# Kernel optimization log

Measured on AMD Instinct MI355X. Metric: run time of the kernel, lower is better.

Reference implementation:

```python
import jax, jax.numpy as jnp
import numpy as np

N, DIM, L = 65536, 128, 8


def setup_inputs() -> dict:
    rng = np.random.default_rng(0)
    # depth-consistent random tree: node 0 is root (depth 0); every other node
    # gets depth in [1, L-1] and a parent chosen uniformly among depth-1 nodes.
    depth = np.zeros(N, dtype=np.int64)
    depth[1:] = rng.integers(1, L, size=N - 1)
    depth = np.sort(depth)  # node 0 stays root; contiguous levels
    parent = np.full(N, N, dtype=np.int64)  # sentinel N for the root (dropped in segment_sum slice)
    for d in range(1, L):
        cur = np.nonzero(depth == d)[0]
        prev = np.nonzero(depth == d - 1)[0]
        parent[cur] = rng.choice(prev, size=cur.size)
    key = jax.random.key(0)
    k = jax.random.split(key, 5)
    s = 1.0 / np.sqrt(DIM)
    return {
        "x": jax.random.normal(k[0], (N, DIM), jnp.float32),
        "parent": jnp.asarray(parent),
        "depth": jnp.asarray(depth),
        "Wioux": jax.random.normal(k[1], (DIM, 3 * DIM), jnp.float32) * s,
        "Wiouh": jax.random.normal(k[2], (DIM, 3 * DIM), jnp.float32) * s,
        "Wfx": jax.random.normal(k[3], (DIM, DIM), jnp.float32) * s,
        "Wfh": jax.random.normal(k[4], (DIM, DIM), jnp.float32) * s,
        "n_levels": L,
    }


def reference(x, parent, depth, Wioux, Wiouh, Wfx, Wfh, n_levels):
    n, dim = x.shape
    xi = x @ Wioux          # [N, 3d]  precomputed input projections
    xf = x @ Wfx            # [N, d]
    pidx = jnp.minimum(parent, n - 1)  # safe gather index (root sentinel clipped; root is never a child)
    h = jnp.zeros_like(x)
    c = jnp.zeros_like(x)
    # process tree bottom-up, one depth level at a time (equivalent to the
    # torch depth-descending per-node loop since children are exactly one level deeper)
    for d in range(int(n_levels) - 1, -1, -1):
        child = depth == d + 1          # nodes that are children of level-d nodes
        cm = child[:, None]
        h_sum = jax.ops.segment_sum(jnp.where(cm, h, 0.0), parent, num_segments=n + 1)[:n]
        n_child = jax.ops.segment_sum(child.astype(x.dtype), parent, num_segments=n + 1)[:n]
        # per-child forget gate: sigmoid(fx(x[parent]) + fh(h_child))
        f = jax.nn.sigmoid(xf[pidx] + h @ Wfh)
        fc_sum = jax.ops.segment_sum(jnp.where(cm, f * c, 0.0), parent, num_segments=n + 1)[:n]
        i_, o_, u_ = jnp.split(xi + h_sum @ Wiouh, 3, axis=-1)
        c_int = fc_sum + jax.nn.sigmoid(i_) * jnp.tanh(u_)
        h_int = jax.nn.sigmoid(o_) * jnp.tanh(c_int)
        leaf = (n_child == 0)[:, None]  # leaves: h = x, c = tanh(x) (as in torch code)
        h_new = jnp.where(leaf, x, h_int)
        c_new = jnp.where(leaf, jnp.tanh(x), c_int)
        lvl = (depth == d)[:, None]
        h = jnp.where(lvl, h_new, h)
        c = jnp.where(lvl, c_new, c)
    return h
```

## Files before the change

kernel.cpp:

```cpp
#include <hip/hip_runtime.h>
#include <hip/hip_bf16.h>

#define DIM 128
#define LVL 8

typedef unsigned int u32;
typedef unsigned short u16;

using bf16x8 = __attribute__((ext_vector_type(8))) short;
using f32x4  = __attribute__((ext_vector_type(4))) float;

__device__ __forceinline__ float bf2f(u16 u) { union { u32 i; float f; } v; v.i = ((u32)u) << 16; return v.f; }
__device__ __forceinline__ u16 f2bf(float f) { __hip_bfloat16 b = __float2bfloat16(f); return *reinterpret_cast<u16*>(&b); }
__device__ __forceinline__ u32 pk2(float lo, float hi) { return (u32)f2bf(lo) | ((u32)f2bf(hi) << 16); }
__device__ __forceinline__ float sigf(float x) { return 1.f / (1.f + __expf(-x)); }
__device__ __forceinline__ float tanhfast(float x) { return 1.f - 2.f / (__expf(2.f * x) + 1.f); }

__global__ void k_levels(const int* __restrict__ depth, int n, int* __restrict__ ofs) {
  int d = threadIdx.x;
  if (d > LVL) return;
  int lo = 0, hi = n;
  while (lo < hi) { int mid = (lo + hi) >> 1; if (depth[mid] < d) lo = mid + 1; else hi = mid; }
  ofs[d] = lo;
}

__global__ void k_mark(const int* __restrict__ parent, int n, int* __restrict__ haschild) {
  int j = blockIdx.x * blockDim.x + threadIdx.x;
  if (j >= n) return;
  int p = parent[j];
  if (p >= 0 && p < n) haschild[p] = 1;
}

__global__ void k_prep(const float* __restrict__ Wioux, const float* __restrict__ Wiouh,
                       const float* __restrict__ Wfx, const float* __restrict__ Wfh,
                       u16* __restrict__ WcT, u16* __restrict__ WhT, u16* __restrict__ WfhT) {
  int i = blockIdx.x * 256 + threadIdx.x;
  if (i >= 1024 * 128) return;
  int c = i >> 7, k = i & 127;
  float v; u16* dst;
  if (c < 512) {
    v = (c < 384) ? Wioux[(size_t)k * 384 + c] : Wfx[(size_t)k * 128 + (c - 384)];
    dst = &WcT[(size_t)c * 128 + k];
  } else if (c < 896) {
    int cc = c - 512; v = Wiouh[(size_t)k * 384 + cc]; dst = &WhT[(size_t)cc * 128 + k];
  } else {
    int cc = c - 896; v = Wfh[(size_t)k * 128 + cc]; dst = &WfhT[(size_t)cc * 128 + k];
  }
  *dst = f2bf(v);
}

__global__ __launch_bounds__(256) void k_big(const float* __restrict__ x, const u16* __restrict__ WcT,
                                             const int* __restrict__ haschild, u16* __restrict__ xi, int n) {
  __shared__ __align__(16) char smem[16384 + 32768];
  char* xsb = smem;
  char* wtb = smem + 16384;
  u16* dbuf = (u16*)(smem + 16384);
  __shared__ int s_any;
  int tid = threadIdx.x;
  int wave = tid >> 6, lane = tid & 63, m = lane & 15, kg = lane >> 4;
  int row0 = blockIdx.x * 64;
  if (tid == 0) {
    int a = 0;
    for (int r = 0; r < 64 && row0 + r < n; ++r) a |= haschild[row0 + r];
    s_any = a;
  }
  __syncthreads();
  if (!s_any) return;
  for (int i = tid; i < 64 * 16; i += 256) {
    int r = i >> 4, c8 = (i & 15) * 8;
    int gr = row0 + r;
    uint4 o = make_uint4(0u, 0u, 0u, 0u);
    if (gr < n) {
      float4 a = *(const float4*)(x + (size_t)gr * DIM + c8);
      float4 b = *(const float4*)(x + (size_t)gr * DIM + c8 + 4);
      o = make_uint4(pk2(a.x, a.y), pk2(a.z, a.w), pk2(b.x, b.y), pk2(b.z, b.w));
    }
    *(uint4*)(xsb + r * 256 + ((c8 * 2) ^ ((r & 7) << 4))) = o;
  }
  int arow = wave * 16 + m;
  uint4 wreg[8];
  #pragma unroll
  for (int j = 0; j < 8; ++j) {
    int i = tid + j * 256;
    wreg[j] = *(const uint4*)(WcT + (size_t)(i >> 4) * 128 + (i & 15) * 8);
  }
  for (int ci = 0; ci < 4; ++ci) {
    __syncthreads();
    #pragma unroll
    for (int j = 0; j < 8; ++j) {
      int i = tid + j * 256;
      int cl = i >> 4, k8 = (i & 15) * 8;
      *(uint4*)(wtb + cl * 256 + ((k8 * 2) ^ ((cl & 7) << 4))) = wreg[j];
    }
    __syncthreads();
    if (ci < 3) {
      #pragma unroll
      for (int j = 0; j < 8; ++j) {
        int i = tid + j * 256;
        wreg[j] = *(const uint4*)(WcT + (size_t)((ci + 1) * 128 + (i >> 4)) * 128 + (i & 15) * 8);
      }
    }
    f32x4 acc[8];
    #pragma unroll
    for (int nt = 0; nt < 8; ++nt) acc[nt] = (f32x4){0.f, 0.f, 0.f, 0.f};
    #pragma unroll
    for (int kk = 0; kk < 4; ++kk) {
      int kbyte = kk * 64 + kg * 16;
      bf16x8 a = *(const bf16x8*)(xsb + arow * 256 + (kbyte ^ ((arow & 7) << 4)));
      #pragma unroll
      for (int nt = 0; nt < 8; ++nt) {
        int col = nt * 16 + m;
        bf16x8 b = *(const bf16x8*)(wtb + col * 256 + (kbyte ^ ((col & 7) << 4)));
        acc[nt] = __builtin_amdgcn_mfma_f32_16x16x32_bf16(a, b, acc[nt], 0, 0, 0);
      }
    }
    __syncthreads();
    #pragma unroll
    for (int nt = 0; nt < 8; ++nt)
      #pragma unroll
      for (int r = 0; r < 4; ++r)
        dbuf[(wave * 16 + kg * 4 + r) * 136 + nt * 16 + m] = f2bf(acc[nt][r]);
    __syncthreads();
    int r2 = tid >> 2, q = tid & 3;
    int gr = row0 + r2;
    if (gr < n && haschild[gr]) {
      const u16* src = dbuf + r2 * 136 + q * 32;
      u16* dst = xi + (size_t)gr * 512 + ci * 128 + q * 32;
      #pragma unroll
      for (int seg = 0; seg < 4; ++seg)
        *(uint4*)(dst + seg * 8) = *(const uint4*)(src + seg * 8);
    }
  }
}

__global__ __launch_bounds__(256) void k_level(const float* __restrict__ x,
    const u16* __restrict__ WhT, const u16* __restrict__ WfhT, const u16* __restrict__ xi,
    const int* __restrict__ haschild, const int* __restrict__ parent,
    const int* __restrict__ ofs, float* __restrict__ hout,
    float* hsum, float* fcsum, int d) {
  __shared__ __align__(16) char smem[16384 + 33792];
  char* hsb = smem;
  char* wtb = smem + 16384;
  float* dbuf = (float*)(smem + 16384);
  __shared__ int ps[64];
  __shared__ int flags[64];
  __shared__ int s_uni, s_anyp;
  int v0 = ofs[d], v1 = ofs[d + 1];
  int tid = threadIdx.x;
  int wave = tid >> 6, lane = tid & 63, m = lane & 15, kg = lane >> 4;
  int arow = wave * 16 + m;
  for (int row0 = v0 + (int)blockIdx.x * 64; row0 < v1; row0 += (int)gridDim.x * 64) {
    int nrows = min(64, v1 - row0);
    if (tid < 64) {
      flags[tid] = (tid < nrows) ? haschild[row0 + tid] : 0;
      ps[tid] = (tid < nrows) ? parent[row0 + tid] : -1;
    }
    __syncthreads();
    if (tid == 0) {
      int a = 0; for (int r = 0; r < 64; ++r) a |= flags[r];
      s_anyp = a;
      int u = 1, p0 = ps[0];
      for (int r = 1; r < nrows; ++r) if (ps[r] != p0) { u = 0; break; }
      s_uni = u;
    }
    __syncthreads();
    f32x4 acc[3][8];
    #pragma unroll
    for (int ci = 0; ci < 3; ++ci)
      #pragma unroll
      for (int nt = 0; nt < 8; ++nt) acc[ci][nt] = (f32x4){0.f, 0.f, 0.f, 0.f};
    if (s_anyp) {
      for (int i = tid; i < 64 * 16; i += 256) {
        int r = i >> 4, c8 = (i & 15) * 8;
        uint4 o = make_uint4(0u, 0u, 0u, 0u);
        if (r < nrows) {
          const float* hp = hsum + (size_t)(row0 + r) * DIM + c8;
          float4 a = *(const float4*)hp; float4 b = *(const float4*)(hp + 4);
          o = make_uint4(pk2(a.x, a.y), pk2(a.z, a.w), pk2(b.x, b.y), pk2(b.z, b.w));
        }
        *(uint4*)(hsb + r * 256 + ((c8 * 2) ^ ((r & 7) << 4))) = o;
      }
      #pragma unroll
      for (int ci = 0; ci < 3; ++ci) {
        for (int i = tid; i < 128 * 16; i += 256) {
          int cl = i >> 4, k8 = (i & 15) * 8;
          uint4 v = *(const uint4*)(WhT + (size_t)(ci * 128 + cl) * 128 + k8);
          *(uint4*)(wtb + cl * 256 + ((k8 * 2) ^ ((cl & 7) << 4))) = v;
        }
        __syncthreads();
        #pragma unroll
        for (int kk = 0; kk < 4; ++kk) {
          int kbyte = kk * 64 + kg * 16;
          bf16x8 a = *(const bf16x8*)(hsb + arow * 256 + (kbyte ^ ((arow & 7) << 4)));
          #pragma unroll
          for (int nt = 0; nt < 8; ++nt) {
            int col = nt * 16 + m;
            bf16x8 b = *(const bf16x8*)(wtb + col * 256 + (kbyte ^ ((col & 7) << 4)));
            acc[ci][nt] = __builtin_amdgcn_mfma_f32_16x16x32_bf16(a, b, acc[ci][nt], 0, 0, 0);
          }
        }
        __syncthreads();
      }
    }
    float cc[8][4];
    #pragma unroll
    for (int nt = 0; nt < 8; ++nt) {
      int col = nt * 16 + m;
      #pragma unroll
      for (int r = 0; r < 4; ++r) {
        int rl = wave * 16 + kg * 4 + r;
        int grow = row0 + rl;
        float hv = 0.f, cv = 0.f;
        if (rl < nrows) {
          bool leaf = (flags[rl] == 0);
          float xv = x[(size_t)grow * DIM + col];
          float iv = bf2f(xi[(size_t)grow * 512 + col])       + acc[0][nt][r];
          float ov = bf2f(xi[(size_t)grow * 512 + 128 + col]) + acc[1][nt][r];
          float uv = bf2f(xi[(size_t)grow * 512 + 256 + col]) + acc[2][nt][r];
          float fcv = fcsum[(size_t)grow * DIM + col];
          float ci_ = fcv + sigf(iv) * tanhfast(uv);
          hv = leaf ? xv : sigf(ov) * tanhfast(ci_);
          cv = leaf ? tanhfast(xv) : ci_;
          hout[(size_t)grow * DIM + col] = hv;
        }
        cc[nt][r] = cv;
        if (d > 0) *(u16*)(hsb + rl * 256 + ((2 * col) ^ ((rl & 7) << 4))) = f2bf(hv);
      }
    }
    if (d > 0) {
      for (int i = tid; i < 128 * 16; i += 256) {
        int cl = i >> 4, k8 = (i & 15) * 8;
        uint4 v = *(const uint4*)(WfhT + (size_t)cl * 128 + k8);
        *(uint4*)(wtb + cl * 256 + ((k8 * 2) ^ ((cl & 7) << 4))) = v;
      }
      __syncthreads();
      f32x4 fp[8];
      #pragma unroll
      for (int nt = 0; nt < 8; ++nt) fp[nt] = (f32x4){0.f, 0.f, 0.f, 0.f};
      #pragma unroll
      for (int kk = 0; kk < 4; ++kk) {
        int kbyte = kk * 64 + kg * 16;
        bf16x8 a = *(const bf16x8*)(hsb + arow * 256 + (kbyte ^ ((arow & 7) << 4)));
        #pragma unroll
        for (int nt = 0; nt < 8; ++nt) {
          int col = nt * 16 + m;
          bf16x8 b = *(const bf16x8*)(wtb + col * 256 + (kbyte ^ ((col & 7) << 4)));
          fp[nt] = __builtin_amdgcn_mfma_f32_16x16x32_bf16(a, b, fp[nt], 0, 0, 0);
        }
      }
      __syncthreads();
      if (s_uni) {
        int p = ps[0];
        #pragma unroll
        for (int nt = 0; nt < 8; ++nt) {
          int col = nt * 16 + m;
          float xfv = bf2f(xi[(size_t)p * 512 + 384 + col]);
          #pragma unroll
          for (int r = 0; r < 4; ++r) {
            int rl = wave * 16 + kg * 4 + r;
            float fc = (rl < nrows) ? sigf(xfv + fp[nt][r]) * cc[nt][r] : 0.f;
            dbuf[rl * 132 + col] = fc;
          }
        }
        __syncthreads();
        if (tid < 128) {
          float sh = 0.f, sf = 0.f;
          for (int r = 0; r < 64; ++r) {
            sh += bf2f(*(const u16*)(hsb + r * 256 + ((2 * tid) ^ ((r & 7) << 4))));
            sf += dbuf[r * 132 + tid];
          }
          atomicAdd(&hsum[(size_t)p * DIM + tid], sh);
          atomicAdd(&fcsum[(size_t)p * DIM + tid], sf);
        }
        __syncthreads();
      } else {
        #pragma unroll
        for (int nt = 0; nt < 8; ++nt) {
          int col = nt * 16 + m;
          #pragma unroll
          for (int r = 0; r < 4; ++r) {
            int rl = wave * 16 + kg * 4 + r;
            if (rl < nrows) {
              int p = ps[rl];
              float xfv = bf2f(xi[(size_t)p * 512 + 384 + col]);
              float fc = sigf(xfv + fp[nt][r]) * cc[nt][r];
              atomicAdd(&fcsum[(size_t)p * DIM + col], fc);
              float hvv = bf2f(*(const u16*)(hsb + rl * 256 + ((2 * col) ^ ((rl & 7) << 4))));
              atomicAdd(&hsum[(size_t)p * DIM + col], hvv);
            }
          }
        }
        __syncthreads();
      }
    } else {
      __syncthreads();
    }
  }
}

extern "C" void kernel_launch(void* const* d_in, const int* in_sizes, int n_in,
                              void* d_out, int out_size, void* d_ws, size_t ws_size,
                              hipStream_t stream) {
  const float* x    = (const float*)d_in[0];
  const int* parent = (const int*)d_in[1];
  const int* depth  = (const int*)d_in[2];
  const float* Wioux = (const float*)d_in[3];
  const float* Wiouh = (const float*)d_in[4];
  const float* Wfx   = (const float*)d_in[5];
  const float* Wfh   = (const float*)d_in[6];
  int n = in_sizes[0] / DIM;
  float* h = (float*)d_out;

  u16*   WcT  = (u16*)d_ws;
  u16*   WhT  = WcT + 512 * 128;
  u16*   WfhT = WhT + 384 * 128;
  u16*   xi   = WfhT + 128 * 128;
  float* hsum = (float*)(xi + (size_t)n * 512);
  float* fcsum = hsum + (size_t)n * DIM;
  int*   haschild = (int*)(fcsum + (size_t)n * DIM);
  int*   ofs  = haschild + n;

  hipMemsetAsync(hsum, 0, (size_t)2 * n * DIM * sizeof(float) + (size_t)n * sizeof(int), stream);
  k_prep<<<512, 256, 0, stream>>>(Wioux, Wiouh, Wfx, Wfh, WcT, WhT, WfhT);
  k_levels<<<1, 32, 0, stream>>>(depth, n, ofs);
  k_mark<<<(n + 255) / 256, 256, 0, stream>>>(parent, n, haschild);
  k_big<<<(n + 63) / 64, 256, 0, stream>>>(x, WcT, haschild, xi, n);

  for (int d = LVL - 1; d >= 0; --d)
    k_level<<<256, 256, 0, stream>>>(x, WhT, WfhT, xi, haschild, parent, ofs, h, hsum, fcsum, d);
}
```

Baseline: 389.9 us.

## Count child degrees to replace memset with selective zeroing and direct single-child writes

Replaces the haschild flags with per-node child counts. The full memset of hsum/fcsum becomes a kernel that zeroes only rows with two or more children, and single-child parents get plain stores instead of atomics. The xi and fcsum layouts are changed so k_big writes MFMA accumulator rows straight to global memory without an LDS staging buffer, and k_level reads them as wide vector loads. The level-0 root is handled by a dedicated single-block kernel. In exchange this adds two extra small kernels, and it depends on the level-1 child count being stored into deg[0] to get the root right.

```diff
diff --git a/kernel.cpp b/kernel.cpp
--- a/kernel.cpp
+++ b/kernel.cpp
@@ -16,19 +16,34 @@
 __device__ __forceinline__ float sigf(float x) { return 1.f / (1.f + __expf(-x)); }
 __device__ __forceinline__ float tanhfast(float x) { return 1.f - 2.f / (__expf(2.f * x) + 1.f); }
 
-__global__ void k_levels(const int* __restrict__ depth, int n, int* __restrict__ ofs) {
+__global__ void k_levels(const int* __restrict__ depth, int n, int* __restrict__ ofs, int* __restrict__ deg) {
   int d = threadIdx.x;
-  if (d > LVL) return;
-  int lo = 0, hi = n;
-  while (lo < hi) { int mid = (lo + hi) >> 1; if (depth[mid] < d) lo = mid + 1; else hi = mid; }
-  ofs[d] = lo;
-}
-
-__global__ void k_mark(const int* __restrict__ parent, int n, int* __restrict__ haschild) {
+  if (d <= LVL) {
+    int lo = 0, hi = n;
+    while (lo < hi) { int mid = (lo + hi) >> 1; if (depth[mid] < d) lo = mid + 1; else hi = mid; }
+    ofs[d] = lo;
+  }
+  __syncthreads();
+  if (d == 0) deg[0] = ofs[2] - ofs[1];
+}
+
+__global__ void k_mark(const int* __restrict__ parent, const int* __restrict__ depth, int n,
+                       int* __restrict__ deg) {
   int j = blockIdx.x * blockDim.x + threadIdx.x;
   if (j >= n) return;
+  if (depth[j] < 2) return;
   int p = parent[j];
-  if (p >= 0 && p < n) haschild[p] = 1;
+  if (p >= 0 && p < n) atomicAdd(&deg[p], 1);
+}
+
+__global__ void k_zero(const int* __restrict__ deg, int n, float* __restrict__ hsum, float* __restrict__ fcsum) {
+  int row = blockIdx.x * 4 + (threadIdx.x >> 6);
+  if (row >= n) return;
+  if (deg[row] < 2) return;
+  int l = threadIdx.x & 63;
+  float2 z; z.x = 0.f; z.y = 0.f;
+  *(float2*)(hsum + (size_t)row * DIM + l * 2) = z;
+  *(float2*)(fcsum + (size_t)row * DIM + l * 2) = z;
 }
 
 __global__ void k_prep(const float* __restrict__ Wioux, const float* __restrict__ Wiouh,
@@ -50,20 +65,18 @@
 }
 
 __global__ __launch_bounds__(256) void k_big(const float* __restrict__ x, const u16* __restrict__ WcT,
-                                             const int* __restrict__ haschild, u16* __restrict__ xi, int n) {
+                                             const int* __restrict__ deg, u16* __restrict__ xi, int n) {
   __shared__ __align__(16) char smem[16384 + 32768];
   char* xsb = smem;
   char* wtb = smem + 16384;
-  u16* dbuf = (u16*)(smem + 16384);
+  __shared__ int flg[64];
   __shared__ int s_any;
   int tid = threadIdx.x;
   int wave = tid >> 6, lane = tid & 63, m = lane & 15, kg = lane >> 4;
   int row0 = blockIdx.x * 64;
-  if (tid == 0) {
-    int a = 0;
-    for (int r = 0; r < 64 && row0 + r < n; ++r) a |= haschild[row0 + r];
-    s_any = a;
-  }
+  if (tid < 64) flg[tid] = (row0 + tid < n) ? (deg[row0 + tid] > 0) : 0;
+  __syncthreads();
+  if (tid == 0) { int a = 0; for (int r = 0; r < 64; ++r) a |= flg[r]; s_any = a; }
   __syncthreads();
   if (!s_any) return;
   for (int i = tid; i < 64 * 16; i += 256) {
@@ -78,28 +91,14 @@
     *(uint4*)(xsb + r * 256 + ((c8 * 2) ^ ((r & 7) << 4))) = o;
   }
   int arow = wave * 16 + m;
-  uint4 wreg[8];
-  #pragma unroll
-  for (int j = 0; j < 8; ++j) {
-    int i = tid + j * 256;
-    wreg[j] = *(const uint4*)(WcT + (size_t)(i >> 4) * 128 + (i & 15) * 8);
-  }
   for (int ci = 0; ci < 4; ++ci) {
-    __syncthreads();
-    #pragma unroll
-    for (int j = 0; j < 8; ++j) {
-      int i = tid + j * 256;
+    if (ci) __syncthreads();
+    for (int i = tid; i < 128 * 16; i += 256) {
       int cl = i >> 4, k8 = (i & 15) * 8;
-      *(uint4*)(wtb + cl * 256 + ((k8 * 2) ^ ((cl & 7) << 4))) = wreg[j];
-    }
-    __syncthreads();
-    if (ci < 3) {
-      #pragma unroll
-      for (int j = 0; j < 8; ++j) {
-        int i = tid + j * 256;
-        wreg[j] = *(const uint4*)(WcT + (size_t)((ci + 1) * 128 + (i >> 4)) * 128 + (i & 15) * 8);
-      }
-    }
+      uint4 v = *(const uint4*)(WcT + (size_t)(ci * 128 + cl) * 128 + k8);
+      *(uint4*)(wtb + cl * 256 + ((k8 * 2) ^ ((cl & 7) << 4))) = v;
+    }
+    __syncthreads();
     f32x4 acc[8];
     #pragma unroll
     for (int nt = 0; nt < 8; ++nt) acc[nt] = (f32x4){0.f, 0.f, 0.f, 0.f};
@@ -114,36 +113,28 @@
         acc[nt] = __builtin_amdgcn_mfma_f32_16x16x32_bf16(a, b, acc[nt], 0, 0, 0);
       }
     }
-    __syncthreads();
-    #pragma unroll
-    for (int nt = 0; nt < 8; ++nt)
-      #pragma unroll
-      for (int r = 0; r < 4; ++r)
-        dbuf[(wave * 16 + kg * 4 + r) * 136 + nt * 16 + m] = f2bf(acc[nt][r]);
-    __syncthreads();
-    int r2 = tid >> 2, q = tid & 3;
-    int gr = row0 + r2;
-    if (gr < n && haschild[gr]) {
-      const u16* src = dbuf + r2 * 136 + q * 32;
-      u16* dst = xi + (size_t)gr * 512 + ci * 128 + q * 32;
-      #pragma unroll
-      for (int seg = 0; seg < 4; ++seg)
-        *(uint4*)(dst + seg * 8) = *(const uint4*)(src + seg * 8);
+    #pragma unroll
+    for (int r = 0; r < 4; ++r) {
+      int rl = wave * 16 + kg * 4 + r;
+      int gr = row0 + rl;
+      if (gr < n && flg[rl]) {
+        uint4 o = make_uint4(pk2(acc[0][r], acc[1][r]), pk2(acc[2][r], acc[3][r]),
+                             pk2(acc[4][r], acc[5][r]), pk2(acc[6][r], acc[7][r]));
+        *(uint4*)(xi + (((size_t)gr * 4 + ci) * 16 + m) * 8) = o;
+      }
     }
   }
 }
 
 __global__ __launch_bounds__(256) void k_level(const float* __restrict__ x,
     const u16* __restrict__ WhT, const u16* __restrict__ WfhT, const u16* __restrict__ xi,
-    const int* __restrict__ haschild, const int* __restrict__ parent,
-    const int* __restrict__ ofs, float* __restrict__ hout,
-    float* hsum, float* fcsum, int d) {
+    const int* __restrict__ deg, const int* __restrict__ parent, const int* __restrict__ ofs,
+    float* __restrict__ hout, float* hsum, float* fcsum, int d) {
   __shared__ __align__(16) char smem[16384 + 33792];
   char* hsb = smem;
   char* wtb = smem + 16384;
   float* dbuf = (float*)(smem + 16384);
-  __shared__ int ps[64];
-  __shared__ int flags[64];
+  __shared__ int ps[64], pdeg[64], flg[64];
   __shared__ int s_uni, s_anyp;
   int v0 = ofs[d], v1 = ofs[d + 1];
   int tid = threadIdx.x;
@@ -152,16 +143,19 @@
   for (int row0 = v0 + (int)blockIdx.x * 64; row0 < v1; row0 += (int)gridDim.x * 64) {
     int nrows = min(64, v1 - row0);
     if (tid < 64) {
-      flags[tid] = (tid < nrows) ? haschild[row0 + tid] : 0;
-      ps[tid] = (tid < nrows) ? parent[row0 + tid] : -1;
+      int ok = tid < nrows;
+      int p = ok ? parent[row0 + tid] : 0;
+      ps[tid] = p;
+      pdeg[tid] = ok ? deg[p] : 0;
+      flg[tid] = ok ? (deg[row0 + tid] > 0) : 0;
     }
     __syncthreads();
     if (tid == 0) {
-      int a = 0; for (int r = 0; r < 64; ++r) a |= flags[r];
+      int a = 0; for (int r = 0; r < nrows; ++r) a |= flg[r];
       s_anyp = a;
       int u = 1, p0 = ps[0];
       for (int r = 1; r < nrows; ++r) if (ps[r] != p0) { u = 0; break; }
-      s_uni = u;
+      s_uni = u && (pdeg[0] >= 2);
     }
     __syncthreads();
     f32x4 acc[3][8];
@@ -204,97 +198,143 @@
     }
     float cc[8][4];
     #pragma unroll
-    for (int nt = 0; nt < 8; ++nt) {
-      int col = nt * 16 + m;
+    for (int r = 0; r < 4; ++r) {
+      int rl = wave * 16 + kg * 4 + r;
+      int grow = row0 + rl;
+      if (rl < nrows) {
+        bool leaf = !flg[rl];
+        uint4 qi = *(const uint4*)(xi + (((size_t)grow * 4 + 0) * 16 + m) * 8);
+        uint4 qo = *(const uint4*)(xi + (((size_t)grow * 4 + 1) * 16 + m) * 8);
+        uint4 qu = *(const uint4*)(xi + (((size_t)grow * 4 + 2) * 16 + m) * 8);
+        float4 fa = *(const float4*)(fcsum + ((size_t)grow * 16 + m) * 8);
+        float4 fb = *(const float4*)(fcsum + ((size_t)grow * 16 + m) * 8 + 4);
+        #pragma unroll
+        for (int nt = 0; nt < 8; ++nt) {
+          int col = nt * 16 + m;
+          float xv = x[(size_t)grow * DIM + col];
+          float iv = bf2f(((const u16*)&qi)[nt]) + acc[0][nt][r];
+          float ov = bf2f(((const u16*)&qo)[nt]) + acc[1][nt][r];
+          float uv = bf2f(((const u16*)&qu)[nt]) + acc[2][nt][r];
+          float fcv = (nt < 4) ? ((const float*)&fa)[nt] : ((const float*)&fb)[nt - 4];
+          float ci_ = fcv + sigf(iv) * tanhfast(uv);
+          float hv = leaf ? xv : sigf(ov) * tanhfast(ci_);
+          float cv = leaf ? tanhfast(xv) : ci_;
+          cc[nt][r] = cv;
+          hout[(size_t)grow * DIM + col] = hv;
+          *(u16*)(hsb + rl * 256 + ((2 * col) ^ ((rl & 7) << 4))) = f2bf(hv);
+        }
+      } else {
+        #pragma unroll
+        for (int nt = 0; nt < 8; ++nt) {
+          cc[nt][r] = 0.f;
+          *(u16*)(hsb + rl * 256 + ((2 * (nt * 16 + m)) ^ ((rl & 7) << 4))) = 0;
+        }
+      }
+    }
+    for (int i = tid; i < 128 * 16; i += 256) {
+      int cl = i >> 4, k8 = (i & 15) * 8;
+      uint4 v = *(const uint4*)(WfhT + (size_t)cl * 128 + k8);
+      *(uint4*)(wtb + cl * 256 + ((k8 * 2) ^ ((cl & 7) << 4))) = v;
+    }
+    __syncthreads();
+    f32x4 fp[8];
+    #pragma unroll
+    for (int nt = 0; nt < 8; ++nt) fp[nt] = (f32x4){0.f, 0.f, 0.f, 0.f};
+    #pragma unroll
+    for (int kk = 0; kk < 4; ++kk) {
+      int kbyte = kk * 64 + kg * 16;
+      bf16x8 a = *(const bf16x8*)(hsb + arow * 256 + (kbyte ^ ((arow & 7) << 4)));
+      #pragma unroll
+      for (int nt = 0; nt < 8; ++nt) {
+        int col = nt * 16 + m;
+        bf16x8 b = *(const bf16x8*)(wtb + col * 256 + (kbyte ^ ((col & 7) << 4)));
+        fp[nt] = __builtin_amdgcn_mfma_f32_16x16x32_bf16(a, b, fp[nt], 0, 0, 0);
+      }
+    }
+    __syncthreads();
+    if (s_uni) {
+      int p0 = ps[0];
+      uint4 qf = *(const uint4*)(xi + (((size_t)p0 * 4 + 3) * 16 + m) * 8);
       #pragma unroll
       for (int r = 0; r < 4; ++r) {
         int rl = wave * 16 + kg * 4 + r;
-        int grow = row0 + rl;
-        float hv = 0.f, cv = 0.f;
-        if (rl < nrows) {
-          bool leaf = (flags[rl] == 0);
-          float xv = x[(size_t)grow * DIM + col];
-          float iv = bf2f(xi[(size_t)grow * 512 + col])       + acc[0][nt][r];
-          float ov = bf2f(xi[(size_t)grow * 512 + 128 + col]) + acc[1][nt][r];
-          float uv = bf2f(xi[(size_t)grow * 512 + 256 + col]) + acc[2][nt][r];
-          float fcv = fcsum[(size_t)grow * DIM + col];
-          float ci_ = fcv + sigf(iv) * tanhfast(uv);
-          hv = leaf ? xv : sigf(ov) * tanhfast(ci_);
-          cv = leaf ? tanhfast(xv) : ci_;
-          hout[(size_t)grow * DIM + col] = hv;
-        }
-        cc[nt][r] = cv;
-        if (d > 0) *(u16*)(hsb + rl * 256 + ((2 * col) ^ ((rl & 7) << 4))) = f2bf(hv);
-      }
-    }
-    if (d > 0) {
-      for (int i = tid; i < 128 * 16; i += 256) {
-        int cl = i >> 4, k8 = (i & 15) * 8;
-        uint4 v = *(const uint4*)(WfhT + (size_t)cl * 128 + k8);
-        *(uint4*)(wtb + cl * 256 + ((k8 * 2) ^ ((cl & 7) << 4))) = v;
+        bool act = rl < nrows;
+        #pragma unroll
+        for (int nt = 0; nt < 8; ++nt) {
+          float fc = act ? sigf(bf2f(((const u16*)&qf)[nt]) + fp[nt][r]) * cc[nt][r] : 0.f;
+          dbuf[rl * 132 + nt * 16 + m] = fc;
+        }
       }
       __syncthreads();
-      f32x4 fp[8];
-      #pragma unroll
-      for (int nt = 0; nt < 8; ++nt) fp[nt] = (f32x4){0.f, 0.f, 0.f, 0.f};
-      #pragma unroll
-      for (int kk = 0; kk < 4; ++kk) {
-        int kbyte = kk * 64 + kg * 16;
-        bf16x8 a = *(const bf16x8*)(hsb + arow * 256 + (kbyte ^ ((arow & 7) << 4)));
+      if (tid < 128) {
+        float sh = 0.f, sf = 0.f;
+        #pragma unroll 8
+        for (int r = 0; r < 64; ++r) {
+          sh += bf2f(*(const u16*)(hsb + r * 256 + ((2 * tid) ^ ((r & 7) << 4))));
+          sf += dbuf[r * 132 + tid];
+        }
+        atomicAdd(&hsum[(size_t)p0 * DIM + tid], sh);
+        atomicAdd(&fcsum[((size_t)p0 * 16 + (tid & 15)) * 8 + (tid >> 4)], sf);
+      }
+    } else {
+      #pragma unroll
+      for (int r = 0; r < 4; ++r) {
+        int rl = wave * 16 + kg * 4 + r;
+        if (rl >= nrows) continue;
+        int p = ps[rl], dg = pdeg[rl];
+        uint4 qf = *(const uint4*)(xi + (((size_t)p * 4 + 3) * 16 + m) * 8);
+        float fcn[8], hv8[8];
         #pragma unroll
         for (int nt = 0; nt < 8; ++nt) {
-          int col = nt * 16 + m;
-          bf16x8 b = *(const bf16x8*)(wtb + col * 256 + (kbyte ^ ((col & 7) << 4)));
-          fp[nt] = __builtin_amdgcn_mfma_f32_16x16x32_bf16(a, b, fp[nt], 0, 0, 0);
-        }
-      }
-      __syncthreads();
-      if (s_uni) {
-        int p = ps[0];
-        #pragma unroll
-        for (int nt = 0; nt < 8; ++nt) {
-          int col = nt * 16 + m;
-          float xfv = bf2f(xi[(size_t)p * 512 + 384 + col]);
+          fcn[nt] = sigf(bf2f(((const u16*)&qf)[nt]) + fp[nt][r]) * cc[nt][r];
+          hv8[nt] = bf2f(*(const u16*)(hsb + rl * 256 + ((2 * (nt * 16 + m)) ^ ((rl & 7) << 4))));
+        }
+        if (dg == 1) {
           #pragma unroll
-          for (int r = 0; r < 4; ++r) {
-            int rl = wave * 16 + kg * 4 + r;
-            float fc = (rl < nrows) ? sigf(xfv + fp[nt][r]) * cc[nt][r] : 0.f;
-            dbuf[rl * 132 + col] = fc;
+          for (int nt = 0; nt < 8; ++nt)
+            hsum[(size_t)p * DIM + nt * 16 + m] = hv8[nt];
+          float4 s0 = make_float4(fcn[0], fcn[1], fcn[2], fcn[3]);
+          float4 s1 = make_float4(fcn[4], fcn[5], fcn[6], fcn[7]);
+          *(float4*)(fcsum + ((size_t)p * 16 + m) * 8) = s0;
+          *(float4*)(fcsum + ((size_t)p * 16 + m) * 8 + 4) = s1;
+        } else {
+          #pragma unroll
+          for (int nt = 0; nt < 8; ++nt) {
+            atomicAdd(&hsum[(size_t)p * DIM + nt * 16 + m], hv8[nt]);
+            atomicAdd(&fcsum[((size_t)p * 16 + m) * 8 + nt], fcn[nt]);
           }
         }
-        __syncthreads();
-        if (tid < 128) {
-          float sh = 0.f, sf = 0.f;
-          for (int r = 0; r < 64; ++r) {
-            sh += bf2f(*(const u16*)(hsb + r * 256 + ((2 * tid) ^ ((r & 7) << 4))));
-            sf += dbuf[r * 132 + tid];
-          }
-          atomicAdd(&hsum[(size_t)p * DIM + tid], sh);
-          atomicAdd(&fcsum[(size_t)p * DIM + tid], sf);
-        }
-        __syncthreads();
-      } else {
-        #pragma unroll
-        for (int nt = 0; nt < 8; ++nt) {
-          int col = nt * 16 + m;
-          #pragma unroll
-          for (int r = 0; r < 4; ++r) {
-            int rl = wave * 16 + kg * 4 + r;
-            if (rl < nrows) {
-              int p = ps[rl];
-              float xfv = bf2f(xi[(size_t)p * 512 + 384 + col]);
-              float fc = sigf(xfv + fp[nt][r]) * cc[nt][r];
-              atomicAdd(&fcsum[(size_t)p * DIM + col], fc);
-              float hvv = bf2f(*(const u16*)(hsb + rl * 256 + ((2 * col) ^ ((rl & 7) << 4))));
-              atomicAdd(&hsum[(size_t)p * DIM + col], hvv);
-            }
-          }
-        }
-        __syncthreads();
-      }
-    } else {
-      __syncthreads();
-    }
+      }
+    }
+    __syncthreads();
+  }
+}
+
+__global__ void k_root(const float* __restrict__ x, const u16* __restrict__ WhT,
+                       const u16* __restrict__ xi, const int* __restrict__ deg,
+                       const float* __restrict__ hsum, const float* __restrict__ fcsum,
+                       float* __restrict__ hout) {
+  __shared__ float hs[128];
+  __shared__ float pre[384];
+  int tid = threadIdx.x;
+  if (deg[0] == 0) { if (tid < 128) hout[tid] = x[tid]; return; }
+  if (tid < 128) hs[tid] = hsum[tid];
+  __syncthreads();
+  for (int c = tid; c < 384; c += 256) {
+    float a = 0.f;
+    const u16* wr = WhT + (size_t)c * 128;
+    for (int k = 0; k < 128; ++k) a += hs[k] * bf2f(wr[k]);
+    pre[c] = a;
+  }
+  __syncthreads();
+  if (tid < 128) {
+    int m = tid & 15, nt = tid >> 4;
+    float iv = bf2f(xi[((size_t)0 * 16 + m) * 8 + nt])   + pre[tid];
+    float ov = bf2f(xi[((size_t)1 * 16 + m) * 8 + nt])   + pre[128 + tid];
+    float uv = bf2f(xi[((size_t)2 * 16 + m) * 8 + nt])   + pre[256 + tid];
+    float fcv = fcsum[((size_t)m) * 8 + nt];
+    float ci_ = fcv + sigf(iv) * tanhfast(uv);
+    hout[tid] = sigf(ov) * tanhfast(ci_);
   }
 }
 
@@ -317,15 +357,17 @@
   u16*   xi   = WfhT + 128 * 128;
   float* hsum = (float*)(xi + (size_t)n * 512);
   float* fcsum = hsum + (size_t)n * DIM;
-  int*   haschild = (int*)(fcsum + (size_t)n * DIM);
-  int*   ofs  = haschild + n;
-
-  hipMemsetAsync(hsum, 0, (size_t)2 * n * DIM * sizeof(float) + (size_t)n * sizeof(int), stream);
+  int*   deg  = (int*)(fcsum + (size_t)n * DIM);
+  int*   ofs  = deg + n;
+
+  hipMemsetAsync(deg, 0, (size_t)n * sizeof(int), stream);
   k_prep<<<512, 256, 0, stream>>>(Wioux, Wiouh, Wfx, Wfh, WcT, WhT, WfhT);
-  k_levels<<<1, 32, 0, stream>>>(depth, n, ofs);
-  k_mark<<<(n + 255) / 256, 256, 0, stream>>>(parent, n, haschild);
-  k_big<<<(n + 63) / 64, 256, 0, stream>>>(x, WcT, haschild, xi, n);
-
-  for (int d = LVL - 1; d >= 0; --d)
-    k_level<<<256, 256, 0, stream>>>(x, WhT, WfhT, xi, haschild, parent, ofs, h, hsum, fcsum, d);
-}
+  k_levels<<<1, 32, 0, stream>>>(depth, n, ofs, deg);
+  k_mark<<<(n + 255) / 256, 256, 0, stream>>>(parent, depth, n, deg);
+  k_zero<<<(n + 3) / 4, 256, 0, stream>>>(deg, n, hsum, fcsum);
+  k_big<<<(n + 63) / 64, 256, 0, stream>>>(x, WcT, deg, xi, n);
+
+  for (int d = LVL - 1; d >= 1; --d)
+    k_level<<<256, 256, 0, stream>>>(x, WhT, WfhT, xi, deg, parent, ofs, h, hsum, fcsum, d);
+  k_root<<<1, 256, 0, stream>>>(x, WhT, xi, deg, hsum, fcsum, h);
+}
```

New measurement: 403.3 us. +3.4%, slower.
